# Performance work log

Measured on AMD Instinct MI355X. Metric: run time of the kernel, lower is better.

Reference implementation:

```python
import jax, jax.numpy as jnp
import numpy as np

B, T, D = 2, 1024, 1024
NH, HD = 16, 64          # attention heads, head dim (D = NH*HD)
M = 16                   # LRU block size
H = D // M               # number of LRU blocks = 64
EPS = 1e-5
ROPE_BASE = 10000.0


def rmsnorm(x, w):
    ms = jnp.mean(x * x, axis=-1, keepdims=True)
    return x * jax.lax.rsqrt(ms + EPS) * w


def rope_tables(t_len, dtype):
    inv_freq = 1.0 / (ROPE_BASE ** (jnp.arange(0, HD, 2, dtype=jnp.float32) / HD))
    freqs = jnp.arange(t_len, dtype=jnp.float32)[:, None] * inv_freq[None, :]  # [T, HD/2]
    emb = jnp.concatenate([freqs, freqs], axis=-1)                              # [T, HD]
    return emb.astype(dtype)


def apply_rope(x, emb):
    # x: [B, T, NH, HD]
    cos = jnp.cos(emb)[None, :, None, :]
    sin = jnp.sin(emb)[None, :, None, :]
    x1, x2 = jnp.split(x, 2, axis=-1)
    return x * cos + jnp.concatenate([-x2, x1], axis=-1) * sin


def setup_inputs() -> dict:
    key = jax.random.key(0)
    ks = jax.random.split(key, 7)
    w = lambda k, shape: jax.random.normal(k, shape, dtype=jnp.float32) * 0.02
    return {
        "x": jax.random.normal(ks[0], (B, T, D), dtype=jnp.float32),
        "attn_norm_w": jnp.ones((D,), jnp.float32),
        "w_qkv": w(ks[1], (D, 3 * D)),
        "w_attn_out": w(ks[2], (D, D)),
        "lru_norm_w": jnp.ones((D,), jnp.float32),
        "w_v": w(ks[3], (D, D)),
        "w_a": w(ks[4], (D, H * M * (M + 1))),
        "w_out_proj": w(ks[5], (D, D)),
    }


def reference(x, attn_norm_w, w_qkv, w_attn_out, lru_norm_w, w_v, w_a, w_out_proj):
    # ---- RoPE causal attention block (residual) ----
    h = rmsnorm(x, attn_norm_w)
    qkv = (h @ w_qkv).reshape(B, T, 3, NH, HD)
    q, k, v = qkv[:, :, 0], qkv[:, :, 1], qkv[:, :, 2]
    emb = rope_tables(T, x.dtype)
    q = apply_rope(q, emb)
    k = apply_rope(k, emb)
    scores = jnp.einsum("bthd,bshd->bhts", q, k) / jnp.sqrt(jnp.asarray(HD, x.dtype))
    causal = jnp.tril(jnp.ones((T, T), dtype=bool))
    scores = jnp.where(causal[None, None], scores, jnp.asarray(-1e30, x.dtype))
    attn = jax.nn.softmax(scores, axis=-1)
    o = jnp.einsum("bhts,bshd->bthd", attn, v).reshape(B, T, D)
    x = x + o @ w_attn_out

    # ---- BlockDiagonalLRU block (residual) ----
    h2 = rmsnorm(x, lru_norm_w)
    vv = (h2 @ w_v).reshape(B, T, H, M)
    gates = jax.nn.softmax((h2 @ w_a).reshape(B, T, H, M, M + 1), axis=-1)
    a0 = gates[..., 0]   # [B, T, H, M]
    A = gates[..., 1:]   # [B, T, H, M, M]

    def step(state, inp):
        A_t, a0_t, v_t = inp  # [B,H,M,M], [B,H,M], [B,H,M]
        new = jnp.einsum("bhij,bhj->bhi", A_t, state) + a0_t * v_t
        return new, new

    init = jnp.zeros((B, H, M), x.dtype)
    _, outs = jax.lax.scan(
        step, init,
        (jnp.moveaxis(A, 1, 0), jnp.moveaxis(a0, 1, 0), jnp.moveaxis(vv, 1, 0)),
    )
    h_out = jnp.moveaxis(outs, 0, 1).reshape(B, T, D)
    return x + h_out @ w_out_proj
```

## Files before the change

kernel.cpp:

```cpp
#include <hip/hip_runtime.h>


typedef unsigned short u16;
typedef unsigned int   u32;
typedef __bf16 bf16x8 __attribute__((ext_vector_type(8)));
typedef float  f32x4  __attribute__((ext_vector_type(4)));

#define B_  2
#define T_  1024
#define D_  1024
#define NH_ 16
#define HD_ 64
#define H_  64
#define M_  16

__device__ __forceinline__ float b2f(u16 u) {
    return __uint_as_float(((u32)u) << 16);
}
__device__ __forceinline__ u16 f2b(float f) {
    u32 u = __float_as_uint(f);
    u32 r = (u + 0x7FFFu + ((u >> 16) & 1u)) >> 16;
    return (u16)r;
}
__device__ __forceinline__ float blo(u32 u) { return __uint_as_float(u << 16); }
__device__ __forceinline__ float bhi(u32 u) { return __uint_as_float(u & 0xFFFF0000u); }

__device__ __forceinline__ void stage16(const void* gp, void* lp) {
    typedef __attribute__((address_space(1))) const unsigned int GU;
    typedef __attribute__((address_space(3))) unsigned int LU;
    __builtin_amdgcn_global_load_lds((GU*)gp, (LU*)lp, 16, 0, 0);
}

template<int BM, int BN, int BK, int MODE, bool TRUNCK, bool CAUSAL, bool SWZ>
__global__ __launch_bounds__(256) void gemm_bt(
    const u16* __restrict__ A, const u16* __restrict__ Bt,
    void* __restrict__ Cout, void* __restrict__ Cout2,
    const float* __restrict__ addend,
    int M, int N, int K, long strideA, long strideB, long strideC)
{
    constexpr int MT = BM / 32;
    constexpr int NT = BN / 32;
    constexpr int KCH = BK / 8;
    const int z  = blockIdx.z;
    int bx = blockIdx.x, by = blockIdx.y;
    if (SWZ) {
        int f = by * gridDim.x + bx;
        int xcd = f & 7, k = f >> 3;
        bx = k % gridDim.x;
        by = xcd * (gridDim.y >> 3) + k / gridDim.x;
    }
    const int m0 = by * BM;
    const int n0 = bx * BN;
    if (CAUSAL && n0 > m0 + BM - 1) return;
    const int Keff = TRUNCK ? (K < m0 + BM ? K : m0 + BM) : K;

    const u16* Ab = A  + (size_t)z * (size_t)strideA;
    const u16* Bb = Bt + (size_t)z * (size_t)strideB;

    __shared__ alignas(16) u16 As[BM * BK];
    __shared__ alignas(16) u16 Bs[BN * BK];

    const int tid  = threadIdx.x;
    const int lane = tid & 63, w = tid >> 6;
    const int wr = w >> 1, wc = w & 1;
    const int quad = lane >> 4, l16 = lane & 15;

    f32x4 acc[MT][NT] = {};

    constexpr int AITER = (BM * BK / 8) / 256;
    constexpr int BITER = (BN * BK / 8) / 256;

    for (int k0 = 0; k0 < Keff; k0 += BK) {
        #pragma unroll
        for (int it = 0; it < AITER; ++it) {
            int c = it * 256 + tid;
            int m = c / KCH, kc = c % KCH;
            stage16(Ab + (size_t)(m0 + m) * K + k0 + kc * 8,
                    &As[(it * 256 + w * 64) * 8]);
        }
        #pragma unroll
        for (int it = 0; it < BITER; ++it) {
            int c = it * 256 + tid;
            int n = c / KCH, kc = c % KCH;
            stage16(Bb + (size_t)(n0 + n) * K + k0 + kc * 8,
                    &Bs[(it * 256 + w * 64) * 8]);
        }
        __syncthreads();

        #pragma unroll
        for (int kk = 0; kk < BK; kk += 32) {
            bf16x8 af[MT], bfr[NT];
            #pragma unroll
            for (int mt = 0; mt < MT; ++mt)
                af[mt] = *(const bf16x8*)&As[(wr * (BM / 2) + mt * 16 + l16) * BK + kk + quad * 8];
            #pragma unroll
            for (int nt = 0; nt < NT; ++nt)
                bfr[nt] = *(const bf16x8*)&Bs[(wc * (BN / 2) + nt * 16 + l16) * BK + kk + quad * 8];
            #pragma unroll
            for (int mt = 0; mt < MT; ++mt)
                #pragma unroll
                for (int nt = 0; nt < NT; ++nt)
                    acc[mt][nt] = __builtin_amdgcn_mfma_f32_16x16x32_bf16(
                        af[mt], bfr[nt], acc[mt][nt], 0, 0, 0);
        }
        __syncthreads();
    }

    #pragma unroll
    for (int mt = 0; mt < MT; ++mt) {
        #pragma unroll
        for (int nt = 0; nt < NT; ++nt) {
            #pragma unroll
            for (int r = 0; r < 4; ++r) {
                int row = m0 + wr * (BM / 2) + mt * 16 + quad * 4 + r;
                int col = n0 + wc * (BN / 2) + nt * 16 + l16;
                float val = acc[mt][nt][r];
                if (MODE == 0) {
                    if (addend) val += addend[(size_t)row * N + col];
                    ((float*)Cout)[(size_t)z * (size_t)strideC + (size_t)row * N + col] = val;
                } else if (MODE == 1) {
                    ((u16*)Cout)[(size_t)z * (size_t)strideC + (size_t)row * N + col] = f2b(val);
                } else if (MODE == 2) {
                    size_t idx = ((size_t)(z >> 4) * T_ + row) * (size_t)D_ + (z & 15) * HD_ + col;
                    ((u16*)Cout)[idx] = f2b(val);
                } else {
                    const int t  = row & (T_ - 1);
                    const int bb = m0 >> 10;
                    const int cg = (n0 >> 4) + wc * (BN / 32) + nt;
                    if (cg >= 1088) {
                        const int hh = cg - 1088;
                        ((float*)Cout2)[(((size_t)(bb * 64 + hh)) * T_ + t) * 16 + l16] = val;
                    } else {
                        const int hh  = cg / 17;
                        const int rem = cg - hh * 17;
                        ((u16*)Cout)[(((size_t)(bb * 64 + hh)) * T_ + t) * 272 + rem * 16 + l16] = f2b(val);
                    }
                }
            }
        }
    }
}

__global__ __launch_bounds__(256) void rmsnorm_k(
    const float* __restrict__ x, const float* __restrict__ w, u16* __restrict__ out)
{
    const int row = blockIdx.x, tid = threadIdx.x;
    float4 v = ((const float4*)(x + (size_t)row * D_))[tid];
    float ss = v.x * v.x + v.y * v.y + v.z * v.z + v.w * v.w;
    #pragma unroll
    for (int o = 32; o >= 1; o >>= 1) ss += __shfl_xor(ss, o, 64);
    __shared__ float red[4];
    if ((tid & 63) == 0) red[tid >> 6] = ss;
    __syncthreads();
    ss = red[0] + red[1] + red[2] + red[3];
    float scale = rsqrtf(ss * (1.0f / D_) + 1e-5f);
    float4 wv = ((const float4*)w)[tid];
    ushort4 o4;
    o4.x = f2b(v.x * scale * wv.x);
    o4.y = f2b(v.y * scale * wv.y);
    o4.z = f2b(v.z * scale * wv.z);
    o4.w = f2b(v.w * scale * wv.w);
    ((ushort4*)(out + (size_t)row * D_))[tid] = o4;
}

__global__ void convT_all(
    const float* __restrict__ wqkv, const float* __restrict__ wao,
    const float* __restrict__ wv,   const float* __restrict__ wa,
    const float* __restrict__ wop,
    u16* __restrict__ wqkvT, u16* __restrict__ waoT,
    u16* __restrict__ waT,   u16* __restrict__ wopT)
{
    const int x = blockIdx.x;
    const float* in; u16* out; int C, xb;
    if (x < 96)       { in = wqkv; out = wqkvT; C = 3072;  xb = x; }
    else if (x < 128) { in = wao;  out = waoT;  C = 1024;  xb = x - 96; }
    else if (x < 160) { in = wv;   out = waT + (size_t)17408 * 1024; C = 1024; xb = x - 128; }
    else if (x < 704) { in = wa;   out = waT;   C = 17408; xb = x - 160; }
    else              { in = wop;  out = wopT;  C = 1024;  xb = x - 704; }
    constexpr int R = 1024;
    __shared__ float tile[32][33];
    const int c0 = xb * 32, r0 = blockIdx.y * 32;
    const int tx = threadIdx.x, ty = threadIdx.y;
    #pragma unroll
    for (int k = 0; k < 4; ++k)
        tile[ty + 8 * k][tx] = in[(size_t)(r0 + ty + 8 * k) * C + c0 + tx];
    __syncthreads();
    #pragma unroll
    for (int k = 0; k < 4; ++k)
        out[(size_t)(c0 + ty + 8 * k) * R + r0 + tx] = f2b(tile[tx][ty + 8 * k]);
}

__global__ void transpose_bf16_k(const u16* __restrict__ in_, u16* __restrict__ out_, int R, int C)
{
    __shared__ u16 tile[32][33];
    const u16* in = in_ + (size_t)blockIdx.z * R * C;
    u16* out      = out_ + (size_t)blockIdx.z * R * C;
    const int c0 = blockIdx.x * 32, r0 = blockIdx.y * 32;
    const int tx = threadIdx.x, ty = threadIdx.y;
    #pragma unroll
    for (int k = 0; k < 4; ++k)
        tile[ty + 8 * k][tx] = in[(size_t)(r0 + ty + 8 * k) * C + c0 + tx];
    __syncthreads();
    #pragma unroll
    for (int k = 0; k < 4; ++k)
        out[(size_t)(c0 + ty + 8 * k) * R + r0 + tx] = tile[tx][ty + 8 * k];
}

__global__ __launch_bounds__(256) void rope_k(
    const float* __restrict__ qkv, u16* __restrict__ Qb, u16* __restrict__ Kb, u16* __restrict__ Vb)
{
    const int bt = blockIdx.x;
    const int b = bt >> 10, t = bt & (T_ - 1);
    const float* row = qkv + (size_t)bt * 3072;
    const int tid = threadIdx.x;
    #pragma unroll
    for (int it = 0; it < 2; ++it) {
        int p = tid + it * 256;
        int h = p >> 5, i = p & 31;
        float ang = (float)t * exp2f(-(float)i * 0.41524101186092034f);
        float sn, cs;
        sincosf(ang, &sn, &cs);
        float q1 = row[h * 64 + i], q2 = row[h * 64 + i + 32];
        float k1 = row[1024 + h * 64 + i], k2 = row[1024 + h * 64 + i + 32];
        size_t ob = ((size_t)(b * NH_ + h) * T_ + t) * HD_ + i;
        Qb[ob]      = f2b(q1 * cs - q2 * sn);
        Qb[ob + 32] = f2b(q2 * cs + q1 * sn);
        Kb[ob]      = f2b(k1 * cs - k2 * sn);
        Kb[ob + 32] = f2b(k2 * cs + k1 * sn);
    }
    #pragma unroll
    for (int it = 0; it < 4; ++it) {
        int d = tid + it * 256;
        int h = d >> 6, i = d & 63;
        Vb[((size_t)(b * NH_ + h) * T_ + t) * HD_ + i] = f2b(row[2048 + d]);
    }
}

__global__ __launch_bounds__(256) void softmax_causal_k(u16* __restrict__ S)
{
    const int w = threadIdx.x >> 6, lane = threadIdx.x & 63;
    const int z = blockIdx.x * 4 + w;
    const int t = z & (T_ - 1);
    u16* row = S + (size_t)z * T_;
    const int n = t + 1;
    const int kmax = (t & ~63) + 64;
    const int kb = lane * 4;
    float v[4][4];
    float mx = -1e30f;
    #pragma unroll
    for (int it = 0; it < 4; ++it) {
        int k = it * 256 + kb;
        if (k < kmax) {
            uint2 d = *(const uint2*)(row + k);
            v[it][0] = (k + 0 < n) ? blo(d.x) * 0.125f : -1e30f;
            v[it][1] = (k + 1 < n) ? bhi(d.x) * 0.125f : -1e30f;
            v[it][2] = (k + 2 < n) ? blo(d.y) * 0.125f : -1e30f;
            v[it][3] = (k + 3 < n) ? bhi(d.y) * 0.125f : -1e30f;
        } else {
            v[it][0] = v[it][1] = v[it][2] = v[it][3] = -1e30f;
        }
        mx = fmaxf(mx, fmaxf(fmaxf(v[it][0], v[it][1]), fmaxf(v[it][2], v[it][3])));
    }
    #pragma unroll
    for (int o = 32; o >= 1; o >>= 1) mx = fmaxf(mx, __shfl_xor(mx, o, 64));
    float sum = 0.f;
    #pragma unroll
    for (int it = 0; it < 4; ++it)
        #pragma unroll
        for (int j = 0; j < 4; ++j) {
            float e = (v[it][j] > -1e29f) ? __expf(v[it][j] - mx) : 0.f;
            v[it][j] = e;
            sum += e;
        }
    #pragma unroll
    for (int o = 32; o >= 1; o >>= 1) sum += __shfl_xor(sum, o, 64);
    float inv = 1.0f / sum;
    #pragma unroll
    for (int it = 0; it < 4; ++it) {
        int k = it * 256 + kb;
        if (k < kmax) {
            uint2 d;
            d.x = (u32)f2b(v[it][0] * inv) | ((u32)f2b(v[it][1] * inv) << 16);
            d.y = (u32)f2b(v[it][2] * inv) | ((u32)f2b(v[it][3] * inv) << 16);
            *(uint2*)(row + k) = d;
        }
    }
}

__device__ __forceinline__ void scan_prep(u16* glds, float* vlds, int lane)
{
    #pragma unroll
    for (int rnd = 0; rnd < 2; ++rnd) {
        float p[4][17];
        #pragma unroll
        for (int j = 0; j < 4; ++j) {
            int r = rnd * 256 + j * 64 + lane;
            const u16* g = &glds[r * 17];
            float vv[17];
            float mx = -1e30f;
            #pragma unroll
            for (int tt = 0; tt < 17; ++tt) { vv[tt] = b2f(g[tt]); mx = fmaxf(mx, vv[tt]); }
            float s = 0.f;
            #pragma unroll
            for (int tt = 0; tt < 17; ++tt) { vv[tt] = __expf(vv[tt] - mx); s += vv[tt]; }
            float inv = 1.0f / s;
            #pragma unroll
            for (int tt = 0; tt < 17; ++tt) p[j][tt] = vv[tt] * inv;
        }
        __syncthreads();
        #pragma unroll
        for (int j = 0; j < 4; ++j) {
            int r = rnd * 256 + j * 64 + lane;
            uint4 w0, w1;
            w0.x = (u32)f2b(p[j][1])  | ((u32)f2b(p[j][2])  << 16);
            w0.y = (u32)f2b(p[j][3])  | ((u32)f2b(p[j][4])  << 16);
            w0.z = (u32)f2b(p[j][5])  | ((u32)f2b(p[j][6])  << 16);
            w0.w = (u32)f2b(p[j][7])  | ((u32)f2b(p[j][8])  << 16);
            w1.x = (u32)f2b(p[j][9])  | ((u32)f2b(p[j][10]) << 16);
            w1.y = (u32)f2b(p[j][11]) | ((u32)f2b(p[j][12]) << 16);
            w1.z = (u32)f2b(p[j][13]) | ((u32)f2b(p[j][14]) << 16);
            w1.w = (u32)f2b(p[j][15]) | ((u32)f2b(p[j][16]) << 16);
            ((uint4*)glds)[r * 2]     = w0;
            ((uint4*)glds)[r * 2 + 1] = w1;
            vlds[r] *= p[j][0];
        }
        __syncthreads();
    }
}

__global__ __launch_bounds__(64) void scan_p1(
    const u16* __restrict__ gates, const float* __restrict__ vvT,
    float* __restrict__ Pmat, float* __restrict__ evec)
{
    const int c = blockIdx.x, chain = blockIdx.y;
    const int lane = threadIdx.x;
    const int i = lane >> 2, q = lane & 3;
    __shared__ alignas(16) u16   glds[32 * 272];
    __shared__ alignas(16) float vlds[32 * 16];
    __shared__ alignas(16) float Pb[2][256];
    __shared__ float slds[16];

    const char* gbase = (const char*)(gates + ((size_t)chain * T_ + c * 32) * 272);
    #pragma unroll
    for (int it = 0; it < 17; ++it)
        stage16(gbase + it * 1024 + lane * 16, (char*)glds + it * 1024);
    const char* vbase = (const char*)(vvT + ((size_t)chain * T_ + c * 32) * 16);
    #pragma unroll
    for (int it = 0; it < 2; ++it)
        stage16(vbase + it * 1024 + lane * 16, (char*)vlds + it * 1024);
    __syncthreads();

    scan_prep(glds, vlds, lane);

    {
        f32x4 idq;
        #pragma unroll
        for (int m = 0; m < 4; ++m) idq[m] = (i == q * 4 + m) ? 1.f : 0.f;
        *(f32x4*)&Pb[0][i * 16 + q * 4] = idq;
    }
    f32x4 e4[4] = {};
    f32x4 np = {};
    float neLast = 0.f;
    int cur = 0;

    for (int st = 0; st < 32; ++st) {
        const uint4* rp = (const uint4*)((const char*)glds + (st * 16 + i) * 32);
        uint4 d0 = rp[0], d1 = rp[1];
        float ar[16];
        ar[0]  = blo(d0.x); ar[1]  = bhi(d0.x);
        ar[2]  = blo(d0.y); ar[3]  = bhi(d0.y);
        ar[4]  = blo(d0.z); ar[5]  = bhi(d0.z);
        ar[6]  = blo(d0.w); ar[7]  = bhi(d0.w);
        ar[8]  = blo(d1.x); ar[9]  = bhi(d1.x);
        ar[10] = blo(d1.y); ar[11] = bhi(d1.y);
        ar[12] = blo(d1.z); ar[13] = bhi(d1.z);
        ar[14] = blo(d1.w); ar[15] = bhi(d1.w);

        f32x4 pk[16];
        #pragma unroll
        for (int k = 0; k < 16; ++k)
            pk[k] = *(const f32x4*)&Pb[cur][k * 16 + q * 4];

        f32x4 a = pk[0] * ar[0];
        #pragma unroll
        for (int k = 1; k < 16; ++k) a += pk[k] * ar[k];
        np = a;

        float ne0 = ar[0] * e4[0][0] + ar[1] * e4[0][1] + ar[2] * e4[0][2] + ar[3] * e4[0][3];
        float ne1 = ar[4] * e4[1][0] + ar[5] * e4[1][1] + ar[6] * e4[1][2] + ar[7] * e4[1][3];
        float ne2 = ar[8] * e4[2][0] + ar[9] * e4[2][1] + ar[10] * e4[2][2] + ar[11] * e4[2][3];
        float ne3 = ar[12] * e4[3][0] + ar[13] * e4[3][1] + ar[14] * e4[3][2] + ar[15] * e4[3][3];
        float ne = (ne0 + ne1) + (ne2 + ne3) + vlds[st * 16 + i];

        *(f32x4*)&Pb[cur ^ 1][i * 16 + q * 4] = np;
        if (q == 0) slds[i] = ne;
        #pragma unroll
        for (int m = 0; m < 4; ++m) e4[m] = *(const f32x4*)&slds[m * 4];
        neLast = ne;
        cur ^= 1;
    }

    float* Pd = Pmat + ((size_t)chain * 32 + c) * 256;
    *(f32x4*)&Pd[i * 16 + q * 4] = np;
    if (q == 0) evec[((size_t)chain * 32 + c) * 16 + i] = neLast;
}

__global__ __launch_bounds__(64) void scan_comb(
    const float* __restrict__ Pmat, const float* __restrict__ evec, float* __restrict__ sIn)
{
    const int chain = blockIdx.x;
    const int lane = threadIdx.x;
    const int i = lane >> 2, q = lane & 3;
    __shared__ alignas(16) float Pl[32 * 256];
    __shared__ alignas(16) float El[32 * 16];
    __shared__ float slds[16];

    const char* Pg = (const char*)(Pmat + (size_t)chain * 32 * 256);
    #pragma unroll
    for (int it = 0; it < 32; ++it)
        stage16(Pg + it * 1024 + lane * 16, (char*)Pl + it * 1024);
    const char* Eg = (const char*)(evec + (size_t)chain * 32 * 16);
    #pragma unroll
    for (int it = 0; it < 2; ++it)
        stage16(Eg + it * 1024 + lane * 16, (char*)El + it * 1024);
    __syncthreads();

    f32x4 s4[4] = {};
    if (q == 0) sIn[((size_t)chain * 32 + 0) * 16 + i] = 0.f;
    for (int cc = 0; cc < 32; ++cc) {
        f32x4 pr[4];
        #pragma unroll
        for (int m = 0; m < 4; ++m)
            pr[m] = *(const f32x4*)&Pl[cc * 256 + i * 16 + m * 4];
        float ne = 0.f;
        #pragma unroll
        for (int k = 0; k < 16; ++k) ne += pr[k >> 2][k & 3] * s4[k >> 2][k & 3];
        ne += El[cc * 16 + i];
        if (q == 0) {
            slds[i] = ne;
            if (cc < 31) sIn[((size_t)chain * 32 + cc + 1) * 16 + i] = ne;
        }
        #pragma unroll
        for (int m = 0; m < 4; ++m) s4[m] = *(const f32x4*)&slds[m * 4];
    }
}

__global__ __launch_bounds__(64) void scan_p2(
    const u16* __restrict__ gates, const float* __restrict__ vvT,
    const float* __restrict__ sIn, u16* __restrict__ hout)
{
    const int c = blockIdx.x, chain = blockIdx.y;
    const int b = chain >> 6, hh = chain & 63;
    const int lane = threadIdx.x;
    const int i = lane >> 2, q = lane & 3;
    __shared__ alignas(16) u16   glds[32 * 272];
    __shared__ alignas(16) float vlds[32 * 16];
    __shared__ float slds[16];

    const char* gbase = (const char*)(gates + ((size_t)chain * T_ + c * 32) * 272);
    #pragma unroll
    for (int it = 0; it < 17; ++it)
        stage16(gbase + it * 1024 + lane * 16, (char*)glds + it * 1024);
    const char* vbase = (const char*)(vvT + ((size_t)chain * T_ + c * 32) * 16);
    #pragma unroll
    for (int it = 0; it < 2; ++it)
        stage16(vbase + it * 1024 + lane * 16, (char*)vlds + it * 1024);
    __syncthreads();

    scan_prep(glds, vlds, lane);

    const float* sp = sIn + ((size_t)chain * 32 + c) * 16;
    f32x4 s4[4];
    #pragma unroll
    for (int m = 0; m < 4; ++m) s4[m] = *(const f32x4*)(sp + m * 4);

    u16* hbase = hout + ((size_t)(b * T_ + c * 32)) * D_ + hh * 16;
    for (int st = 0; st < 32; ++st) {
        const uint4* rp = (const uint4*)((const char*)glds + (st * 16 + i) * 32);
        uint4 d0 = rp[0], d1 = rp[1];
        float ne0 = blo(d0.x) * s4[0][0] + bhi(d0.x) * s4[0][1]
                  + blo(d0.y) * s4[0][2] + bhi(d0.y) * s4[0][3];
        float ne1 = blo(d0.z) * s4[1][0] + bhi(d0.z) * s4[1][1]
                  + blo(d0.w) * s4[1][2] + bhi(d0.w) * s4[1][3];
        float ne2 = blo(d1.x) * s4[2][0] + bhi(d1.x) * s4[2][1]
                  + blo(d1.y) * s4[2][2] + bhi(d1.y) * s4[2][3];
        float ne3 = blo(d1.z) * s4[3][0] + bhi(d1.z) * s4[3][1]
                  + blo(d1.w) * s4[3][2] + bhi(d1.w) * s4[3][3];
        float ne = (ne0 + ne1) + (ne2 + ne3) + vlds[st * 16 + i];
        if (q == 0) {
            slds[i] = ne;
            hbase[(size_t)st * D_ + i] = f2b(ne);
        }
        #pragma unroll
        for (int m = 0; m < 4; ++m) s4[m] = *(const f32x4*)&slds[m * 4];
    }
}

extern "C" void kernel_launch(void* const* d_in, const int* in_sizes, int n_in,
                              void* d_out, int out_size, void* d_ws, size_t ws_size,
                              hipStream_t stream)
{
    const float* x    = (const float*)d_in[0];
    const float* anw  = (const float*)d_in[1];
    const float* wqkv = (const float*)d_in[2];
    const float* wao  = (const float*)d_in[3];
    const float* lnw  = (const float*)d_in[4];
    const float* wv   = (const float*)d_in[5];
    const float* wa   = (const float*)d_in[6];
    const float* wop  = (const float*)d_in[7];

    char* ws = (char*)d_ws;
    const size_t MB = 1u << 20;
    u16*   h     = (u16*)  (ws +   0 * MB);
    u16*   h2    = (u16*)  (ws +   4 * MB);
    u16*   wqkvT = (u16*)  (ws +   8 * MB);
    u16*   waoT  = (u16*)  (ws +  14 * MB);
    u16*   wopT  = (u16*)  (ws +  16 * MB);
    u16*   waT   = (u16*)  (ws +  18 * MB);
    float* qkvf  = (float*)(ws +  54 * MB);
    float* x2    = (float*)(ws +  54 * MB);
    float* vvT   = (float*)(ws +  62 * MB);
    u16*   Qb    = (u16*)  (ws +  78 * MB);
    float* Pmat  = (float*)(ws +  78 * MB);
    u16*   Kb    = (u16*)  (ws +  82 * MB);
    float* evec  = (float*)(ws +  82 * MB);
    float* sIn   = (float*)(ws +  82 * MB + 256 * 1024);
    u16*   Vb    = (u16*)  (ws +  86 * MB);
    u16*   Vt    = (u16*)  (ws +  90 * MB);
    u16*   S     = (u16*)  (ws +  94 * MB);
    u16*   omat  = (u16*)  (ws + 158 * MB);
    u16*   gates = (u16*)  (ws +  94 * MB);
    u16*   hout  = (u16*)  (ws + 162 * MB);
    (void)in_sizes; (void)n_in; (void)out_size; (void)ws_size;

    dim3 tb(32, 8);
    convT_all<<<dim3(736, 32), tb, 0, stream>>>(
        wqkv, wao, wv, wa, wop, wqkvT, waoT, waT, wopT);

    rmsnorm_k<<<2048, 256, 0, stream>>>(x, anw, h);
    gemm_bt<64, 128, 32, 0, false, false, false><<<dim3(24, 32, 1), 256, 0, stream>>>(
        h, wqkvT, (void*)qkvf, nullptr, nullptr, 2048, 3072, 1024, 0, 0, 0);
    rope_k<<<2048, 256, 0, stream>>>(qkvf, Qb, Kb, Vb);
    transpose_bf16_k<<<dim3(2, 32, 32), tb, 0, stream>>>(Vb, Vt, 1024, 64);

    gemm_bt<128, 128, 64, 1, false, true, false><<<dim3(8, 8, 32), 256, 0, stream>>>(
        Qb, Kb, (void*)S, nullptr, nullptr, 1024, 1024, 64, 65536, 65536, 1048576);
    softmax_causal_k<<<8192, 256, 0, stream>>>(S);
    gemm_bt<64, 64, 64, 2, true, false, false><<<dim3(1, 16, 32), 256, 0, stream>>>(
        S, Vt, (void*)omat, nullptr, nullptr, 1024, 64, 1024, 1048576, 65536, 0);

    gemm_bt<64, 128, 32, 0, false, false, false><<<dim3(8, 32, 1), 256, 0, stream>>>(
        omat, waoT, (void*)x2, nullptr, x, 2048, 1024, 1024, 0, 0, 0);
    rmsnorm_k<<<2048, 256, 0, stream>>>(x2, lnw, h2);

    gemm_bt<128, 128, 32, 5, false, false, true><<<dim3(144, 16, 1), 256, 0, stream>>>(
        h2, waT, (void*)gates, (void*)vvT, nullptr, 2048, 18432, 1024, 0, 0, 0);

    scan_p1<<<dim3(32, 128), 64, 0, stream>>>(gates, vvT, Pmat, evec);
    scan_comb<<<128, 64, 0, stream>>>(Pmat, evec, sIn);
    scan_p2<<<dim3(32, 128), 64, 0, stream>>>(gates, vvT, sIn, hout);

    gemm_bt<64, 128, 32, 0, false, false, false><<<dim3(8, 32, 1), 256, 0, stream>>>(
        hout, wopT, d_out, nullptr, x2, 2048, 1024, 1024, 0, 0, 0);
}
```

Before: 505.3 us.

## Fuse RoPE and QKV head-split into QKV GEMM epilogue; rework gate GEMM swizzle

```diff
diff --git a/kernel.cpp b/kernel.cpp
--- a/kernel.cpp
+++ b/kernel.cpp
@@ -31,10 +31,10 @@
     __builtin_amdgcn_global_load_lds((GU*)gp, (LU*)lp, 16, 0, 0);
 }
 
-template<int BM, int BN, int BK, int MODE, bool TRUNCK, bool CAUSAL, bool SWZ>
+template<int BM, int BN, int BK, int MODE, bool TRUNCK, bool CAUSAL, int SWZ>
 __global__ __launch_bounds__(256) void gemm_bt(
     const u16* __restrict__ A, const u16* __restrict__ Bt,
-    void* __restrict__ Cout, void* __restrict__ Cout2,
+    void* __restrict__ Cout, void* __restrict__ Cout2, void* __restrict__ Cout3,
     const float* __restrict__ addend,
     int M, int N, int K, long strideA, long strideB, long strideC)
 {
@@ -43,11 +43,11 @@
     constexpr int KCH = BK / 8;
     const int z  = blockIdx.z;
     int bx = blockIdx.x, by = blockIdx.y;
-    if (SWZ) {
+    if (SWZ == 2) {
         int f = by * gridDim.x + bx;
         int xcd = f & 7, k = f >> 3;
-        bx = k % gridDim.x;
-        by = xcd * (gridDim.y >> 3) + k / gridDim.x;
+        by = k & 15;
+        bx = xcd * (gridDim.x >> 3) + (k >> 4);
     }
     const int m0 = by * BM;
     const int n0 = bx * BN;
@@ -106,6 +106,37 @@
         __syncthreads();
     }
 
+    if (MODE == 6) {
+        const int reg = n0 >> 10;
+        const int hh  = ((n0 & 1023) >> 6) + wc;
+        #pragma unroll
+        for (int mt = 0; mt < MT; ++mt) {
+            #pragma unroll
+            for (int r = 0; r < 4; ++r) {
+                int row = m0 + wr * (BM / 2) + mt * 16 + quad * 4 + r;
+                int t = row & (T_ - 1), bb = row >> 10;
+                size_t obase = ((size_t)(bb * NH_ + hh) * T_ + t) * HD_;
+                if (reg == 2) {
+                    #pragma unroll
+                    for (int nt = 0; nt < 4; ++nt)
+                        ((u16*)Cout3)[obase + nt * 16 + l16] = f2b(acc[mt][nt][r]);
+                } else {
+                    u16* dst = (reg == 0) ? (u16*)Cout : (u16*)Cout2;
+                    #pragma unroll
+                    for (int nt = 0; nt < 2; ++nt) {
+                        int i = nt * 16 + l16;
+                        float ang = (float)t * exp2f(-(float)i * 0.41524101186092034f);
+                        float sn, cs;
+                        sincosf(ang, &sn, &cs);
+                        float q1 = acc[mt][nt][r], q2 = acc[mt][nt + 2][r];
+                        dst[obase + i]      = f2b(q1 * cs - q2 * sn);
+                        dst[obase + i + 32] = f2b(q2 * cs + q1 * sn);
+                    }
+                }
+            }
+        }
+        return;
+    }
     #pragma unroll
     for (int mt = 0; mt < MT; ++mt) {
         #pragma unroll
@@ -206,36 +237,6 @@
         out[(size_t)(c0 + ty + 8 * k) * R + r0 + tx] = tile[tx][ty + 8 * k];
 }
 
-__global__ __launch_bounds__(256) void rope_k(
-    const float* __restrict__ qkv, u16* __restrict__ Qb, u16* __restrict__ Kb, u16* __restrict__ Vb)
-{
-    const int bt = blockIdx.x;
-    const int b = bt >> 10, t = bt & (T_ - 1);
-    const float* row = qkv + (size_t)bt * 3072;
-    const int tid = threadIdx.x;
-    #pragma unroll
-    for (int it = 0; it < 2; ++it) {
-        int p = tid + it * 256;
-        int h = p >> 5, i = p & 31;
-        float ang = (float)t * exp2f(-(float)i * 0.41524101186092034f);
-        float sn, cs;
-        sincosf(ang, &sn, &cs);
-        float q1 = row[h * 64 + i], q2 = row[h * 64 + i + 32];
-        float k1 = row[1024 + h * 64 + i], k2 = row[1024 + h * 64 + i + 32];
-        size_t ob = ((size_t)(b * NH_ + h) * T_ + t) * HD_ + i;
-        Qb[ob]      = f2b(q1 * cs - q2 * sn);
-        Qb[ob + 32] = f2b(q2 * cs + q1 * sn);
-        Kb[ob]      = f2b(k1 * cs - k2 * sn);
-        Kb[ob + 32] = f2b(k2 * cs + k1 * sn);
-    }
-    #pragma unroll
-    for (int it = 0; it < 4; ++it) {
-        int d = tid + it * 256;
-        int h = d >> 6, i = d & 63;
-        Vb[((size_t)(b * NH_ + h) * T_ + t) * HD_ + i] = f2b(row[2048 + d]);
-    }
-}
-
 __global__ __launch_bounds__(256) void softmax_causal_k(u16* __restrict__ S)
 {
     const int w = threadIdx.x >> 6, lane = threadIdx.x & 63;
@@ -517,7 +518,6 @@
     u16*   waoT  = (u16*)  (ws +  14 * MB);
     u16*   wopT  = (u16*)  (ws +  16 * MB);
     u16*   waT   = (u16*)  (ws +  18 * MB);
-    float* qkvf  = (float*)(ws +  54 * MB);
     float* x2    = (float*)(ws +  54 * MB);
     float* vvT   = (float*)(ws +  62 * MB);
     u16*   Qb    = (u16*)  (ws +  78 * MB);
@@ -538,28 +538,27 @@
         wqkv, wao, wv, wa, wop, wqkvT, waoT, waT, wopT);
 
     rmsnorm_k<<<2048, 256, 0, stream>>>(x, anw, h);
-    gemm_bt<64, 128, 32, 0, false, false, false><<<dim3(24, 32, 1), 256, 0, stream>>>(
-        h, wqkvT, (void*)qkvf, nullptr, nullptr, 2048, 3072, 1024, 0, 0, 0);
-    rope_k<<<2048, 256, 0, stream>>>(qkvf, Qb, Kb, Vb);
+    gemm_bt<64, 128, 32, 6, false, false, 0><<<dim3(24, 32, 1), 256, 0, stream>>>(
+        h, wqkvT, (void*)Qb, (void*)Kb, (void*)Vb, nullptr, 2048, 3072, 1024, 0, 0, 0);
     transpose_bf16_k<<<dim3(2, 32, 32), tb, 0, stream>>>(Vb, Vt, 1024, 64);
 
-    gemm_bt<128, 128, 64, 1, false, true, false><<<dim3(8, 8, 32), 256, 0, stream>>>(
-        Qb, Kb, (void*)S, nullptr, nullptr, 1024, 1024, 64, 65536, 65536, 1048576);
+    gemm_bt<128, 128, 64, 1, false, true, 0><<<dim3(8, 8, 32), 256, 0, stream>>>(
+        Qb, Kb, (void*)S, nullptr, nullptr, nullptr, 1024, 1024, 64, 65536, 65536, 1048576);
     softmax_causal_k<<<8192, 256, 0, stream>>>(S);
-    gemm_bt<64, 64, 64, 2, true, false, false><<<dim3(1, 16, 32), 256, 0, stream>>>(
-        S, Vt, (void*)omat, nullptr, nullptr, 1024, 64, 1024, 1048576, 65536, 0);
-
-    gemm_bt<64, 128, 32, 0, false, false, false><<<dim3(8, 32, 1), 256, 0, stream>>>(
-        omat, waoT, (void*)x2, nullptr, x, 2048, 1024, 1024, 0, 0, 0);
+    gemm_bt<64, 64, 64, 2, true, false, 0><<<dim3(1, 16, 32), 256, 0, stream>>>(
+        S, Vt, (void*)omat, nullptr, nullptr, nullptr, 1024, 64, 1024, 1048576, 65536, 0);
+
+    gemm_bt<64, 128, 32, 0, false, false, 0><<<dim3(8, 32, 1), 256, 0, stream>>>(
+        omat, waoT, (void*)x2, nullptr, nullptr, x, 2048, 1024, 1024, 0, 0, 0);
     rmsnorm_k<<<2048, 256, 0, stream>>>(x2, lnw, h2);
 
-    gemm_bt<128, 128, 32, 5, false, false, true><<<dim3(144, 16, 1), 256, 0, stream>>>(
-        h2, waT, (void*)gates, (void*)vvT, nullptr, 2048, 18432, 1024, 0, 0, 0);
+    gemm_bt<128, 128, 32, 5, false, false, 2><<<dim3(144, 16, 1), 256, 0, stream>>>(
+        h2, waT, (void*)gates, (void*)vvT, nullptr, nullptr, 2048, 18432, 1024, 0, 0, 0);
 
     scan_p1<<<dim3(32, 128), 64, 0, stream>>>(gates, vvT, Pmat, evec);
     scan_comb<<<128, 64, 0, stream>>>(Pmat, evec, sIn);
     scan_p2<<<dim3(32, 128), 64, 0, stream>>>(gates, vvT, sIn, hout);
 
-    gemm_bt<64, 128, 32, 0, false, false, false><<<dim3(8, 32, 1), 256, 0, stream>>>(
-        hout, wopT, d_out, nullptr, x2, 2048, 1024, 1024, 0, 0, 0);
-}
+    gemm_bt<64, 128, 32, 0, false, false, 0><<<dim3(8, 32, 1), 256, 0, stream>>>(
+        hout, wopT, d_out, nullptr, nullptr, x2, 2048, 1024, 1024, 0, 0, 0);
+}
```

Measured after the change: 492.6 us. 2.5% less time.
